# Kernel optimization log

Measured on AMD Instinct MI355X. Metric: run time of the kernel, lower is better.

The kernel has to match this reference:

```python
import jax, jax.numpy as jnp
import numpy as np

B, NF, H, W, D, S = 32, 16, 8, 24, 256, 21
NUM_ACTOR = 20
EPS = 1e-8      # slot-attention eps
LN_EPS = 1e-5   # torch LayerNorm default


def _ln(x, g, b):
    m = x.mean(-1, keepdims=True)
    v = ((x - m) ** 2).mean(-1, keepdims=True)
    return (x - m) / jnp.sqrt(v + LN_EPS) * g + b


def setup_inputs() -> dict:
    key = jax.random.key(0)
    ks = jax.random.split(key, 12)
    s = 1.0 / np.sqrt(D)
    lin = lambda k: jax.random.normal(k, (D, D), jnp.float32) * s
    return {
        "inputs": jax.random.normal(ks[0], (B, NF, H, W, D), jnp.float32),
        "noise": jax.random.normal(ks[1], (B, S, D), jnp.float32),
        "slots_mu": jax.random.normal(ks[2], (1, 1, D), jnp.float32),
        "slots_sigma": jnp.abs(jax.random.normal(ks[3], (1, 1, D), jnp.float32)),
        "Wq": lin(ks[4]), "bq": jnp.zeros(D, jnp.float32),
        "Wk": lin(ks[5]), "bk": jnp.zeros(D, jnp.float32),
        "Wv": lin(ks[6]), "bv": jnp.zeros(D, jnp.float32),
        "W1": lin(ks[7]), "b1": jnp.zeros(D, jnp.float32),
        "W2": lin(ks[8]), "b2": jnp.zeros(D, jnp.float32),
        "W_ih": jax.random.normal(ks[9], (3 * D, D), jnp.float32) * s,
        "b_ih": jnp.zeros(3 * D, jnp.float32),
        "W_hh": jax.random.normal(ks[10], (3 * D, D), jnp.float32) * s,
        "b_hh": jnp.zeros(3 * D, jnp.float32),
        "g_in": jnp.ones(D, jnp.float32), "be_in": jnp.zeros(D, jnp.float32),
        "g_sl": jnp.ones(D, jnp.float32), "be_sl": jnp.zeros(D, jnp.float32),
        "g_ff": jnp.ones(D, jnp.float32), "be_ff": jnp.zeros(D, jnp.float32),
    }


def reference(inputs, noise, slots_mu, slots_sigma, Wq, bq, Wk, bk, Wv, bv,
              W1, b1, W2, b2, W_ih, b_ih, W_hh, b_hh,
              g_in, be_in, g_sl, be_sl, g_ff, be_ff):
    scale = D ** -0.5
    slots0 = slots_mu + slots_sigma * noise  # [B,S,D]

    def gru(x, h):  # torch.nn.GRUCell math; x,h: [B*S, D]
        gi = x @ W_ih.T + b_ih
        gh = h @ W_hh.T + b_hh
        ir, iz, inn = jnp.split(gi, 3, axis=-1)
        hr, hz, hn = jnp.split(gh, 3, axis=-1)
        r = jax.nn.sigmoid(ir + hr)
        z = jax.nn.sigmoid(iz + hz)
        n = jnp.tanh(inn + r * hn)
        return (1.0 - z) * n + z * h

    def iterate(slots, k, v):
        q = _ln(slots, g_sl, be_sl) @ Wq.T + bq            # [B,S,D]
        dots = jnp.einsum('bid,bjd->bij', q, k) * scale    # [B,S,N]
        attn_ori = jax.nn.softmax(dots, axis=1) + EPS      # softmax over SLOT axis
        attn = attn_ori / attn_ori.sum(-1, keepdims=True)
        updates = jnp.einsum('bjd,bij->bid', v, attn)      # [B,S,D]
        h = gru(updates.reshape(-1, D), slots.reshape(-1, D)).reshape(B, S, D)
        slots_new = h + jax.nn.relu(_ln(h, g_ff, be_ff) @ W1.T + b1) @ W2.T + b2
        return slots_new, attn_ori

    def frame_step(slots, frame):  # frame: [B,H,W,D]
        x = _ln(frame.reshape(B, H * W, D), g_in, be_in)
        k = x @ Wk.T + bk
        v = x @ Wv.T + bv
        attn = None
        for _ in range(3):  # fixed 3 slot-attention iterations per frame
            slots, attn = iterate(slots, k, v)
        return slots, (slots, attn)

    frames = jnp.moveaxis(inputs, 1, 0)  # [NF,B,H,W,D]
    _, (slots_stack, attn_stack) = jax.lax.scan(frame_step, slots0, frames)
    slots_out = slots_stack[-1][:, :NUM_ACTOR, :]   # last frame, first 20 slots
    attns = jnp.moveaxis(attn_stack, 0, 1)          # [B,NF,S,N]
    return slots_out, attns
```

## Files before the change

### kernel.cpp

```cpp
#include <hip/hip_runtime.h>


typedef _Float16 f16;
typedef _Float16 half8 __attribute__((ext_vector_type(8)));
typedef float floatx4 __attribute__((ext_vector_type(4)));

#define WQ_OFF 0
#define WKT_OFF 16384
#define WV_OFF 32768
#define W1_OFF 49152
#define W2_OFF 65536
#define WIH_OFF 81920
#define WHH_OFF 131072
__device__ __align__(16) uint4 g_wpk[180224];

__device__ inline float wredsum(float v) {
#pragma unroll
  for (int m = 32; m > 0; m >>= 1) v += __shfl_xor(v, m, 64);
  return v;
}
__device__ inline float fsigmoid(float x) { return 1.f / (1.f + __expf(-x)); }
__device__ inline float ftanh(float x) {
  float ax = fabsf(x);
  float e = __expf(-2.f * ax);
  return copysignf((1.f - e) / (1.f + e), x);
}

__device__ inline floatx4 mfma16(half8 a, half8 b, floatx4 c) {
  return __builtin_amdgcn_mfma_f32_16x16x32_f16(a, b, c, 0, 0, 0);
}
__device__ inline void zero8(half8& a) {
#pragma unroll
  for (int e = 0; e < 8; e++) a[e] = (f16)0.f;
}
__device__ inline void split8(const float* __restrict__ p, half8& hi, half8& lo) {
  float4 v0 = *(const float4*)p;
  float4 v1 = *(const float4*)(p + 4);
  float vv[8] = {v0.x, v0.y, v0.z, v0.w, v1.x, v1.y, v1.z, v1.w};
#pragma unroll
  for (int e = 0; e < 8; e++) {
    f16 h = (f16)vv[e];
    hi[e] = h;
    lo[e] = (f16)(vv[e] - (float)h);
  }
}

__device__ inline void mfma_gemm_acc(const float* __restrict__ Ain, int woff, int tid,
                                     floatx4 acc[4]) {
  const int l = tid & 63, wv = tid >> 6;
  const int mt = wv & 1, ntb = (wv >> 1) * 4, lq = l >> 4, lr = l & 15;
  const int row = mt * 16 + lr;
  const bool rv = row < 21;
  const float* arow = Ain + row * 256;
  for (int ks = 0; ks < 8; ks++) {
    const int k0 = ks * 32 + lq * 8;
    half8 ahi, alo;
    if (rv) split8(arow + k0, ahi, alo);
    else { zero8(ahi); zero8(alo); }
#pragma unroll
    for (int t = 0; t < 4; t++) {
      const int col = (ntb + t) * 16 + lr;
      const uint4* bp = g_wpk + woff + ((col << 5) + (ks << 2) + lq) * 2;
      union { uint4 u; half8 h; } bh, bl;
      bh.u = bp[0]; bl.u = bp[1];
      acc[t] = mfma16(ahi, bh.h, acc[t]);
      acc[t] = mfma16(alo, bh.h, acc[t]);
      acc[t] = mfma16(ahi, bl.h, acc[t]);
    }
  }
}

__device__ inline void mfma_gemm_store(float* __restrict__ Out, const floatx4 acc[4],
                                       const float* __restrict__ bias, bool relu, int tid) {
  const int l = tid & 63, wv = tid >> 6;
  const int mt = wv & 1, ntb = (wv >> 1) * 4, lq = l >> 4, lr = l & 15;
#pragma unroll
  for (int t = 0; t < 4; t++) {
    const int col = (ntb + t) * 16 + lr;
    const float bb = bias ? bias[col] : 0.f;
#pragma unroll
    for (int r = 0; r < 4; r++) {
      const int i = mt * 16 + lq * 4 + r;
      if (i < 21) {
        float v = acc[t][r] + bb;
        Out[i * 256 + col] = relu ? fmaxf(v, 0.f) : v;
      }
    }
  }
}

__global__ __launch_bounds__(1024) void k_prep(
    const float* __restrict__ Wq, const float* __restrict__ Wk, const float* __restrict__ Wv,
    const float* __restrict__ W1, const float* __restrict__ W2,
    const float* __restrict__ Wih, const float* __restrict__ Whh) {
  int t = blockIdx.x * 1024 + threadIdx.x;
  if (t >= 90112) return;
  const float* src;
  int idx;
  bool tr = false;
  if (t < 8192) { src = Wq; idx = t; }
  else if (t < 16384) { src = Wk; idx = t - 8192; tr = true; }
  else if (t < 24576) { src = Wv; idx = t - 16384; }
  else if (t < 32768) { src = W1; idx = t - 24576; }
  else if (t < 40960) { src = W2; idx = t - 32768; }
  else if (t < 65536) { src = Wih; idx = t - 40960; }
  else { src = Whh; idx = t - 65536; }
  int c = idx >> 5, ko = idx & 31;
  union { uint4 u; f16 h[8]; } H, L;
#pragma unroll
  for (int e = 0; e < 8; e++) {
    int k = ko * 8 + e;
    float v = tr ? src[(size_t)k * 256 + c] : src[(size_t)c * 256 + k];
    f16 hi = (f16)v;
    H.h[e] = hi;
    L.h[e] = (f16)(v - (float)hi);
  }
  g_wpk[(size_t)t * 2] = H.u;
  g_wpk[(size_t)t * 2 + 1] = L.u;
}

__global__ __launch_bounds__(512) void k_all(
    const float* __restrict__ x, const float* __restrict__ noise,
    const float* __restrict__ mu, const float* __restrict__ sigma,
    const float* __restrict__ bq, const float* __restrict__ bk,
    const float* __restrict__ bv, const float* __restrict__ b1,
    const float* __restrict__ b2, const float* __restrict__ bih,
    const float* __restrict__ bhh,
    const float* __restrict__ g_in, const float* __restrict__ be_in,
    const float* __restrict__ g_sl, const float* __restrict__ be_sl,
    const float* __restrict__ g_ff, const float* __restrict__ be_ff,
    float* __restrict__ out_slots, float* __restrict__ out_attn) {
  __shared__ f16 LX[256 * 193];
  __shared__ alignas(16) float SL[21 * 256];
  __shared__ alignas(16) float A[21 * 256];
  __shared__ alignas(16) float Bf[21 * 256];
  __shared__ float qb[21], rsum[21];

  const int b = blockIdx.x;
  const int tid = threadIdx.x;
  const int w = tid >> 6, lane = tid & 63;
  const int d = tid & 255;
  const int half = tid >> 8;
  const int i0 = half * 11;
  const int ni = 11 - half;
  const floatx4 vzero = {0.f, 0.f, 0.f, 0.f};

  for (int i = tid; i < 21 * 256; i += 512) {
    int s = i >> 8, dd = i & 255;
    SL[i] = mu[dd] + sigma[dd] * noise[((size_t)b * 21 + s) * 256 + dd];
  }
  __syncthreads();

  for (int f = 0; f < 16; ++f) {
    const float* xf = x + ((size_t)(b * 16 + f)) * 192 * 256;
    for (int rr = 0; rr < 24; rr++) {
      int row = w + rr * 8;
      float4 xv = *(const float4*)(xf + row * 256 + lane * 4);
      float m = wredsum(xv.x + xv.y + xv.z + xv.w) * (1.f / 256.f);
      float d0 = xv.x - m, d1 = xv.y - m, d2 = xv.z - m, d3 = xv.w - m;
      float q2 = wredsum(d0 * d0 + d1 * d1 + d2 * d2 + d3 * d3);
      float rs = 1.f / sqrtf(q2 * (1.f / 256.f) + 1e-5f);
      int c = lane * 4;
      LX[(c + 0) * 193 + row] = (f16)(d0 * rs * g_in[c + 0] + be_in[c + 0]);
      LX[(c + 1) * 193 + row] = (f16)(d1 * rs * g_in[c + 1] + be_in[c + 1]);
      LX[(c + 2) * 193 + row] = (f16)(d2 * rs * g_in[c + 2] + be_in[c + 2]);
      LX[(c + 3) * 193 + row] = (f16)(d3 * rs * g_in[c + 3] + be_in[c + 3]);
    }
    __syncthreads();

    for (int it = 0; it < 3; ++it) {
#pragma unroll
      for (int rr = 0; rr < 3; rr++) {
        int row = w + rr * 8;
        if (row < 21) {
          float4 xv = *(const float4*)(SL + row * 256 + lane * 4);
          float m = wredsum(xv.x + xv.y + xv.z + xv.w) * (1.f / 256.f);
          float d0 = xv.x - m, d1 = xv.y - m, d2 = xv.z - m, d3 = xv.w - m;
          float q2 = wredsum(d0 * d0 + d1 * d1 + d2 * d2 + d3 * d3);
          float rs = 1.f / sqrtf(q2 * (1.f / 256.f) + 1e-5f);
          int c = lane * 4;
          A[row * 256 + c + 0] = d0 * rs * g_sl[c + 0] + be_sl[c + 0];
          A[row * 256 + c + 1] = d1 * rs * g_sl[c + 1] + be_sl[c + 1];
          A[row * 256 + c + 2] = d2 * rs * g_sl[c + 2] + be_sl[c + 2];
          A[row * 256 + c + 3] = d3 * rs * g_sl[c + 3] + be_sl[c + 3];
        }
      }
      __syncthreads();
      {
        floatx4 acc[4] = {vzero, vzero, vzero, vzero};
        mfma_gemm_acc(A, WQ_OFF, tid, acc);
        mfma_gemm_store(Bf, acc, bq, false, tid);
      }
      __syncthreads();
      {
        floatx4 acc[4] = {vzero, vzero, vzero, vzero};
        mfma_gemm_acc(Bf, WKT_OFF, tid, acc);
        mfma_gemm_store(A, acc, nullptr, false, tid);
        if (tid < 336) {
          int i = tid >> 4, p = tid & 15;
          const float* qrow = Bf + i * 256 + p * 16;
          float s = 0.f;
#pragma unroll
          for (int t2 = 0; t2 < 16; t2++) s += qrow[t2] * bk[p * 16 + t2];
          s += __shfl_xor(s, 1, 64);
          s += __shfl_xor(s, 2, 64);
          s += __shfl_xor(s, 4, 64);
          s += __shfl_xor(s, 8, 64);
          if (p == 0) qb[i] = s;
        }
      }
      __syncthreads();
      for (int c = 0; c < 8; c++) {
        int o = tid + (c << 9);
        if (o < 4032) {
          int i = o / 192, j = o - i * 192;
          float s = 0.f;
          for (int k = 0; k < 256; k += 4) {
            float4 q4 = *(const float4*)(A + i * 256 + k);
            s += q4.x * (float)LX[(k + 0) * 193 + j];
            s += q4.y * (float)LX[(k + 1) * 193 + j];
            s += q4.z * (float)LX[(k + 2) * 193 + j];
            s += q4.w * (float)LX[(k + 3) * 193 + j];
          }
          Bf[i * 256 + j] = (s + qb[i]) * 0.0625f;
        }
      }
      __syncthreads();
      if (tid < 192) {
        int j = tid;
        float mx = -1e30f;
#pragma unroll
        for (int i = 0; i < 21; i++) mx = fmaxf(mx, Bf[i * 256 + j]);
        float e[21], sum = 0.f;
#pragma unroll
        for (int i = 0; i < 21; i++) { e[i] = __expf(Bf[i * 256 + j] - mx); sum += e[i]; }
        float inv = 1.f / sum;
#pragma unroll
        for (int i = 0; i < 21; i++) Bf[i * 256 + j] = e[i] * inv + 1e-8f;
      }
      __syncthreads();
#pragma unroll
      for (int q3 = 0; q3 < 3; q3++) {
        int i = w * 3 + q3;
        if (i < 21) {
          float s = Bf[i * 256 + lane] + Bf[i * 256 + lane + 64] + Bf[i * 256 + lane + 128];
          s = wredsum(s);
          if (lane == 0) rsum[i] = s;
        }
      }
      __syncthreads();
      {
        float* oa = out_attn + ((size_t)(b * 16 + f)) * 4032;
        for (int idx = tid; idx < 4032; idx += 512) {
          int i = idx / 192, j = idx - i * 192;
          float ao = Bf[i * 256 + j];
          if (it == 2) oa[idx] = ao;
          Bf[i * 256 + j] = ao / rsum[i];
        }
      }
      __syncthreads();
      {
        float acc[11];
#pragma unroll
        for (int ii = 0; ii < 11; ii++) acc[ii] = 0.f;
        for (int j = 0; j < 192; j += 4) {
          float l0 = (float)LX[d * 193 + j + 0];
          float l1 = (float)LX[d * 193 + j + 1];
          float l2 = (float)LX[d * 193 + j + 2];
          float l3 = (float)LX[d * 193 + j + 3];
#pragma unroll
          for (int ii = 0; ii < 11; ii++)
            if (ii < ni) {
              float4 at = *(const float4*)(Bf + (i0 + ii) * 256 + j);
              acc[ii] += at.x * l0 + at.y * l1 + at.z * l2 + at.w * l3;
            }
        }
#pragma unroll
        for (int ii = 0; ii < 11; ii++)
          if (ii < ni) A[(i0 + ii) * 256 + d] = acc[ii];
      }
      __syncthreads();
      {
        floatx4 acc[4] = {vzero, vzero, vzero, vzero};
        mfma_gemm_acc(A, WV_OFF, tid, acc);
        mfma_gemm_store(Bf, acc, bv, false, tid);
      }
      __syncthreads();
      {
        const int l = tid & 63, wv = tid >> 6;
        const int mt = wv & 1, dtb = (wv >> 1) * 4, lq = l >> 4, lr = l & 15;
        const int row = mt * 16 + lr;
        const bool rv = row < 21;
        const float* urow = Bf + row * 256;
        const float* srow = SL + row * 256;
        for (int p = 0; p < 2; p++) {
          floatx4 aih[2][3], ahh[2][3];
#pragma unroll
          for (int gi = 0; gi < 2; gi++)
#pragma unroll
            for (int g = 0; g < 3; g++) { aih[gi][g] = vzero; ahh[gi][g] = vzero; }
          for (int ks = 0; ks < 8; ks++) {
            const int k0 = ks * 32 + lq * 8;
            half8 uhi, ulo, shi, slo;
            if (rv) { split8(urow + k0, uhi, ulo); split8(srow + k0, shi, slo); }
            else { zero8(uhi); zero8(ulo); zero8(shi); zero8(slo); }
#pragma unroll
            for (int gi = 0; gi < 2; gi++) {
              const int dt = dtb + p * 2 + gi;
#pragma unroll
              for (int g = 0; g < 3; g++) {
                const int colI = g * 256 + dt * 16 + lr;
                const uint4* bp = g_wpk + WIH_OFF + ((colI << 5) + (ks << 2) + lq) * 2;
                union { uint4 u; half8 h; } bh, bl;
                bh.u = bp[0]; bl.u = bp[1];
                aih[gi][g] = mfma16(uhi, bh.h, aih[gi][g]);
                aih[gi][g] = mfma16(ulo, bh.h, aih[gi][g]);
                aih[gi][g] = mfma16(uhi, bl.h, aih[gi][g]);
                const uint4* bp2 = g_wpk + WHH_OFF + ((colI << 5) + (ks << 2) + lq) * 2;
                bh.u = bp2[0]; bl.u = bp2[1];
                ahh[gi][g] = mfma16(shi, bh.h, ahh[gi][g]);
                ahh[gi][g] = mfma16(slo, bh.h, ahh[gi][g]);
                ahh[gi][g] = mfma16(shi, bl.h, ahh[gi][g]);
              }
            }
          }
#pragma unroll
          for (int gi = 0; gi < 2; gi++) {
            const int dt = dtb + p * 2 + gi;
            const int dd = dt * 16 + lr;
            const float bihr = bih[dd], bihz = bih[256 + dd], bihn = bih[512 + dd];
            const float bhhr = bhh[dd], bhhz = bhh[256 + dd], bhhn = bhh[512 + dd];
#pragma unroll
            for (int r = 0; r < 4; r++) {
              const int i = mt * 16 + lq * 4 + r;
              if (i < 21) {
                float rg = fsigmoid(aih[gi][0][r] + ahh[gi][0][r] + bihr + bhhr);
                float zg = fsigmoid(aih[gi][1][r] + ahh[gi][1][r] + bihz + bhhz);
                float ng = ftanh(aih[gi][2][r] + bihn + rg * (ahh[gi][2][r] + bhhn));
                A[i * 256 + dd] = (1.f - zg) * ng + zg * SL[i * 256 + dd];
              }
            }
          }
        }
      }
      __syncthreads();
#pragma unroll
      for (int rr = 0; rr < 3; rr++) {
        int row = w + rr * 8;
        if (row < 21) {
          float4 xv = *(const float4*)(A + row * 256 + lane * 4);
          float m = wredsum(xv.x + xv.y + xv.z + xv.w) * (1.f / 256.f);
          float d0 = xv.x - m, d1 = xv.y - m, d2 = xv.z - m, d3 = xv.w - m;
          float q2 = wredsum(d0 * d0 + d1 * d1 + d2 * d2 + d3 * d3);
          float rs = 1.f / sqrtf(q2 * (1.f / 256.f) + 1e-5f);
          int c = lane * 4;
          Bf[row * 256 + c + 0] = d0 * rs * g_ff[c + 0] + be_ff[c + 0];
          Bf[row * 256 + c + 1] = d1 * rs * g_ff[c + 1] + be_ff[c + 1];
          Bf[row * 256 + c + 2] = d2 * rs * g_ff[c + 2] + be_ff[c + 2];
          Bf[row * 256 + c + 3] = d3 * rs * g_ff[c + 3] + be_ff[c + 3];
        }
      }
      __syncthreads();
      {
        floatx4 acc[4] = {vzero, vzero, vzero, vzero};
        mfma_gemm_acc(Bf, W1_OFF, tid, acc);
        mfma_gemm_store(SL, acc, b1, true, tid);
      }
      __syncthreads();
      {
        floatx4 acc[4] = {vzero, vzero, vzero, vzero};
        mfma_gemm_acc(SL, W2_OFF, tid, acc);
        __syncthreads();
        const int l = tid & 63, wv = tid >> 6;
        const int mt = wv & 1, ntb = (wv >> 1) * 4, lq = l >> 4, lr = l & 15;
#pragma unroll
        for (int t = 0; t < 4; t++) {
          const int col = (ntb + t) * 16 + lr;
          const float bb = b2[col];
#pragma unroll
          for (int r = 0; r < 4; r++) {
            const int i = mt * 16 + lq * 4 + r;
            if (i < 21) SL[i * 256 + col] = A[i * 256 + col] + acc[t][r] + bb;
          }
        }
      }
      __syncthreads();
    }
  }
  for (int i = tid; i < 20 * 256; i += 512) {
    int s = i >> 8, dd = i & 255;
    out_slots[((size_t)b * 20 + s) * 256 + dd] = SL[s * 256 + dd];
  }
}

extern "C" void kernel_launch(void* const* d_in, const int* in_sizes, int n_in,
                              void* d_out, int out_size, void* d_ws, size_t ws_size,
                              hipStream_t stream) {
  const float* inputs = (const float*)d_in[0];
  const float* noise = (const float*)d_in[1];
  const float* mu = (const float*)d_in[2];
  const float* sigma = (const float*)d_in[3];
  const float* Wq = (const float*)d_in[4];
  const float* bq = (const float*)d_in[5];
  const float* Wk = (const float*)d_in[6];
  const float* bk = (const float*)d_in[7];
  const float* Wv = (const float*)d_in[8];
  const float* bv = (const float*)d_in[9];
  const float* W1 = (const float*)d_in[10];
  const float* b1 = (const float*)d_in[11];
  const float* W2 = (const float*)d_in[12];
  const float* b2 = (const float*)d_in[13];
  const float* Wih = (const float*)d_in[14];
  const float* bih = (const float*)d_in[15];
  const float* Whh = (const float*)d_in[16];
  const float* bhh = (const float*)d_in[17];
  const float* g_in = (const float*)d_in[18];
  const float* be_in = (const float*)d_in[19];
  const float* g_sl = (const float*)d_in[20];
  const float* be_sl = (const float*)d_in[21];
  const float* g_ff = (const float*)d_in[22];
  const float* be_ff = (const float*)d_in[23];

  float* out_slots = (float*)d_out;
  float* out_attn = out_slots + 32 * 20 * 256;

  k_prep<<<88, 1024, 0, stream>>>(Wq, Wk, Wv, W1, W2, Wih, Whh);
  k_all<<<32, 512, 0, stream>>>(inputs, noise, mu, sigma, bq, bk, bv, b1, b2,
                                bih, bhh, g_in, be_in, g_sl, be_sl, g_ff, be_ff,
                                out_slots, out_attn);
}
```

Before: 10.85 ms.

## Move attention dot and weighted-sum products to MFMA with padded LDS rows

The per-iteration dots computation (slots x 192 tokens over 256 features) and the attn-weighted sum of normalized inputs are rewritten from scalar FMA loops into 16x16x32 f16 MFMA tiles. The A operand is split into hi/lo halves, and the B fragments are gathered from the transposed LX buffer in LDS. Slot buffers are padded to a row stride of 258 to reduce LDS bank conflicts, and the qb/rsum scratch values are stored in the padding columns. The gathered B fragments read LDS element by element, and the padded stride limits vector loads to float2.

```diff
diff --git a/kernel.cpp b/kernel.cpp
--- a/kernel.cpp
+++ b/kernel.cpp
@@ -4,6 +4,8 @@
 typedef _Float16 f16;
 typedef _Float16 half8 __attribute__((ext_vector_type(8)));
 typedef float floatx4 __attribute__((ext_vector_type(4)));
+
+#define SSTR 258
 
 #define WQ_OFF 0
 #define WKT_OFF 16384
@@ -33,10 +35,12 @@
 #pragma unroll
   for (int e = 0; e < 8; e++) a[e] = (f16)0.f;
 }
-__device__ inline void split8(const float* __restrict__ p, half8& hi, half8& lo) {
-  float4 v0 = *(const float4*)p;
-  float4 v1 = *(const float4*)(p + 4);
-  float vv[8] = {v0.x, v0.y, v0.z, v0.w, v1.x, v1.y, v1.z, v1.w};
+__device__ inline void split8s(const float* __restrict__ p, half8& hi, half8& lo) {
+  float2 a = *(const float2*)(p);
+  float2 b = *(const float2*)(p + 2);
+  float2 c = *(const float2*)(p + 4);
+  float2 d = *(const float2*)(p + 6);
+  float vv[8] = {a.x, a.y, b.x, b.y, c.x, c.y, d.x, d.y};
 #pragma unroll
   for (int e = 0; e < 8; e++) {
     f16 h = (f16)vv[e];
@@ -51,11 +55,11 @@
   const int mt = wv & 1, ntb = (wv >> 1) * 4, lq = l >> 4, lr = l & 15;
   const int row = mt * 16 + lr;
   const bool rv = row < 21;
-  const float* arow = Ain + row * 256;
+  const float* arow = Ain + row * SSTR;
   for (int ks = 0; ks < 8; ks++) {
     const int k0 = ks * 32 + lq * 8;
     half8 ahi, alo;
-    if (rv) split8(arow + k0, ahi, alo);
+    if (rv) split8s(arow + k0, ahi, alo);
     else { zero8(ahi); zero8(alo); }
 #pragma unroll
     for (int t = 0; t < 4; t++) {
@@ -83,7 +87,7 @@
       const int i = mt * 16 + lq * 4 + r;
       if (i < 21) {
         float v = acc[t][r] + bb;
-        Out[i * 256 + col] = relu ? fmaxf(v, 0.f) : v;
+        Out[i * SSTR + col] = relu ? fmaxf(v, 0.f) : v;
       }
     }
   }
@@ -131,23 +135,19 @@
     const float* __restrict__ g_ff, const float* __restrict__ be_ff,
     float* __restrict__ out_slots, float* __restrict__ out_attn) {
   __shared__ f16 LX[256 * 193];
-  __shared__ alignas(16) float SL[21 * 256];
-  __shared__ alignas(16) float A[21 * 256];
-  __shared__ alignas(16) float Bf[21 * 256];
-  __shared__ float qb[21], rsum[21];
+  __shared__ float FBUF[3 * 21 * SSTR];
+  float* SL = FBUF;
+  float* A = FBUF + 21 * SSTR;
+  float* Bf = FBUF + 2 * 21 * SSTR;
 
   const int b = blockIdx.x;
   const int tid = threadIdx.x;
   const int w = tid >> 6, lane = tid & 63;
-  const int d = tid & 255;
-  const int half = tid >> 8;
-  const int i0 = half * 11;
-  const int ni = 11 - half;
   const floatx4 vzero = {0.f, 0.f, 0.f, 0.f};
 
   for (int i = tid; i < 21 * 256; i += 512) {
     int s = i >> 8, dd = i & 255;
-    SL[i] = mu[dd] + sigma[dd] * noise[((size_t)b * 21 + s) * 256 + dd];
+    SL[s * SSTR + dd] = mu[dd] + sigma[dd] * noise[((size_t)b * 21 + s) * 256 + dd];
   }
   __syncthreads();
 
@@ -173,16 +173,18 @@
       for (int rr = 0; rr < 3; rr++) {
         int row = w + rr * 8;
         if (row < 21) {
-          float4 xv = *(const float4*)(SL + row * 256 + lane * 4);
-          float m = wredsum(xv.x + xv.y + xv.z + xv.w) * (1.f / 256.f);
-          float d0 = xv.x - m, d1 = xv.y - m, d2 = xv.z - m, d3 = xv.w - m;
+          const float* sr = SL + row * SSTR + lane * 4;
+          float2 xa = *(const float2*)(sr);
+          float2 xb = *(const float2*)(sr + 2);
+          float m = wredsum(xa.x + xa.y + xb.x + xb.y) * (1.f / 256.f);
+          float d0 = xa.x - m, d1 = xa.y - m, d2 = xb.x - m, d3 = xb.y - m;
           float q2 = wredsum(d0 * d0 + d1 * d1 + d2 * d2 + d3 * d3);
           float rs = 1.f / sqrtf(q2 * (1.f / 256.f) + 1e-5f);
           int c = lane * 4;
-          A[row * 256 + c + 0] = d0 * rs * g_sl[c + 0] + be_sl[c + 0];
-          A[row * 256 + c + 1] = d1 * rs * g_sl[c + 1] + be_sl[c + 1];
-          A[row * 256 + c + 2] = d2 * rs * g_sl[c + 2] + be_sl[c + 2];
-          A[row * 256 + c + 3] = d3 * rs * g_sl[c + 3] + be_sl[c + 3];
+          A[row * SSTR + c + 0] = d0 * rs * g_sl[c + 0] + be_sl[c + 0];
+          A[row * SSTR + c + 1] = d1 * rs * g_sl[c + 1] + be_sl[c + 1];
+          A[row * SSTR + c + 2] = d2 * rs * g_sl[c + 2] + be_sl[c + 2];
+          A[row * SSTR + c + 3] = d3 * rs * g_sl[c + 3] + be_sl[c + 3];
         }
       }
       __syncthreads();
@@ -198,7 +200,7 @@
         mfma_gemm_store(A, acc, nullptr, false, tid);
         if (tid < 336) {
           int i = tid >> 4, p = tid & 15;
-          const float* qrow = Bf + i * 256 + p * 16;
+          const float* qrow = Bf + i * SSTR + p * 16;
           float s = 0.f;
 #pragma unroll
           for (int t2 = 0; t2 < 16; t2++) s += qrow[t2] * bk[p * 16 + t2];
@@ -206,23 +208,40 @@
           s += __shfl_xor(s, 2, 64);
           s += __shfl_xor(s, 4, 64);
           s += __shfl_xor(s, 8, 64);
-          if (p == 0) qb[i] = s;
-        }
-      }
-      __syncthreads();
-      for (int c = 0; c < 8; c++) {
-        int o = tid + (c << 9);
-        if (o < 4032) {
-          int i = o / 192, j = o - i * 192;
-          float s = 0.f;
-          for (int k = 0; k < 256; k += 4) {
-            float4 q4 = *(const float4*)(A + i * 256 + k);
-            s += q4.x * (float)LX[(k + 0) * 193 + j];
-            s += q4.y * (float)LX[(k + 1) * 193 + j];
-            s += q4.z * (float)LX[(k + 2) * 193 + j];
-            s += q4.w * (float)LX[(k + 3) * 193 + j];
-          }
-          Bf[i * 256 + j] = (s + qb[i]) * 0.0625f;
+          if (p == 0) A[i * SSTR + 256] = s;
+        }
+      }
+      __syncthreads();
+      {
+        const int l = tid & 63, wv = tid >> 6;
+        const int mt = wv & 1, jtb = (wv >> 1) * 3, lq = l >> 4, lr = l & 15;
+        const int row = mt * 16 + lr;
+        const bool rv = row < 21;
+        const float* arow = A + row * SSTR;
+        floatx4 acc[3] = {vzero, vzero, vzero};
+        for (int ks = 0; ks < 8; ks++) {
+          const int k0 = ks * 32 + lq * 8;
+          half8 ahi, alo;
+          if (rv) split8s(arow + k0, ahi, alo);
+          else { zero8(ahi); zero8(alo); }
+#pragma unroll
+          for (int t = 0; t < 3; t++) {
+            const int j = (jtb + t) * 16 + lr;
+            half8 bfr;
+#pragma unroll
+            for (int e = 0; e < 8; e++) bfr[e] = LX[(k0 + e) * 193 + j];
+            acc[t] = mfma16(ahi, bfr, acc[t]);
+            acc[t] = mfma16(alo, bfr, acc[t]);
+          }
+        }
+#pragma unroll
+        for (int t = 0; t < 3; t++) {
+          const int j = (jtb + t) * 16 + lr;
+#pragma unroll
+          for (int r = 0; r < 4; r++) {
+            const int i = mt * 16 + lq * 4 + r;
+            if (i < 21) Bf[i * SSTR + j] = (acc[t][r] + A[i * SSTR + 256]) * 0.0625f;
+          }
         }
       }
       __syncthreads();
@@ -230,22 +249,22 @@
         int j = tid;
         float mx = -1e30f;
 #pragma unroll
-        for (int i = 0; i < 21; i++) mx = fmaxf(mx, Bf[i * 256 + j]);
+        for (int i = 0; i < 21; i++) mx = fmaxf(mx, Bf[i * SSTR + j]);
         float e[21], sum = 0.f;
 #pragma unroll
-        for (int i = 0; i < 21; i++) { e[i] = __expf(Bf[i * 256 + j] - mx); sum += e[i]; }
+        for (int i = 0; i < 21; i++) { e[i] = __expf(Bf[i * SSTR + j] - mx); sum += e[i]; }
         float inv = 1.f / sum;
 #pragma unroll
-        for (int i = 0; i < 21; i++) Bf[i * 256 + j] = e[i] * inv + 1e-8f;
+        for (int i = 0; i < 21; i++) Bf[i * SSTR + j] = e[i] * inv + 1e-8f;
       }
       __syncthreads();
 #pragma unroll
       for (int q3 = 0; q3 < 3; q3++) {
         int i = w * 3 + q3;
         if (i < 21) {
-          float s = Bf[i * 256 + lane] + Bf[i * 256 + lane + 64] + Bf[i * 256 + lane + 128];
+          float s = Bf[i * SSTR + lane] + Bf[i * SSTR + lane + 64] + Bf[i * SSTR + lane + 128];
           s = wredsum(s);
-          if (lane == 0) rsum[i] = s;
+          if (lane == 0) A[i * SSTR + 257] = s;
         }
       }
       __syncthreads();
@@ -253,37 +272,10 @@
         float* oa = out_attn + ((size_t)(b * 16 + f)) * 4032;
         for (int idx = tid; idx < 4032; idx += 512) {
           int i = idx / 192, j = idx - i * 192;
-          float ao = Bf[i * 256 + j];
+          float ao = Bf[i * SSTR + j];
           if (it == 2) oa[idx] = ao;
-          Bf[i * 256 + j] = ao / rsum[i];
-        }
-      }
-      __syncthreads();
-      {
-        float acc[11];
-#pragma unroll
-        for (int ii = 0; ii < 11; ii++) acc[ii] = 0.f;
-        for (int j = 0; j < 192; j += 4) {
-          float l0 = (float)LX[d * 193 + j + 0];
-          float l1 = (float)LX[d * 193 + j + 1];
-          float l2 = (float)LX[d * 193 + j + 2];
-          float l3 = (float)LX[d * 193 + j + 3];
-#pragma unroll
-          for (int ii = 0; ii < 11; ii++)
-            if (ii < ni) {
-              float4 at = *(const float4*)(Bf + (i0 + ii) * 256 + j);
-              acc[ii] += at.x * l0 + at.y * l1 + at.z * l2 + at.w * l3;
-            }
-        }
-#pragma unroll
-        for (int ii = 0; ii < 11; ii++)
-          if (ii < ni) A[(i0 + ii) * 256 + d] = acc[ii];
-      }
-      __syncthreads();
-      {
-        floatx4 acc[4] = {vzero, vzero, vzero, vzero};
-        mfma_gemm_acc(A, WV_OFF, tid, acc);
-        mfma_gemm_store(Bf, acc, bv, false, tid);
+          Bf[i * SSTR + j] = ao / A[i * SSTR + 257];
+        }
       }
       __syncthreads();
       {
@@ -291,8 +283,47 @@
         const int mt = wv & 1, dtb = (wv >> 1) * 4, lq = l >> 4, lr = l & 15;
         const int row = mt * 16 + lr;
         const bool rv = row < 21;
-        const float* urow = Bf + row * 256;
-        const float* srow = SL + row * 256;
+        const float* arow = Bf + row * SSTR;
+        floatx4 acc[4] = {vzero, vzero, vzero, vzero};
+        for (int ks = 0; ks < 6; ks++) {
+          const int k0 = ks * 32 + lq * 8;
+          half8 ahi, alo;
+          if (rv) split8s(arow + k0, ahi, alo);
+          else { zero8(ahi); zero8(alo); }
+#pragma unroll
+          for (int t = 0; t < 4; t++) {
+            const int dd = (dtb + t) * 16 + lr;
+            half8 bfr;
+#pragma unroll
+            for (int e = 0; e < 8; e++) bfr[e] = LX[dd * 193 + k0 + e];
+            acc[t] = mfma16(ahi, bfr, acc[t]);
+            acc[t] = mfma16(alo, bfr, acc[t]);
+          }
+        }
+#pragma unroll
+        for (int t = 0; t < 4; t++) {
+          const int dd = (dtb + t) * 16 + lr;
+#pragma unroll
+          for (int r = 0; r < 4; r++) {
+            const int i = mt * 16 + lq * 4 + r;
+            if (i < 21) A[i * SSTR + dd] = acc[t][r];
+          }
+        }
+      }
+      __syncthreads();
+      {
+        floatx4 acc[4] = {vzero, vzero, vzero, vzero};
+        mfma_gemm_acc(A, WV_OFF, tid, acc);
+        mfma_gemm_store(Bf, acc, bv, false, tid);
+      }
+      __syncthreads();
+      {
+        const int l = tid & 63, wv = tid >> 6;
+        const int mt = wv & 1, dtb = (wv >> 1) * 4, lq = l >> 4, lr = l & 15;
+        const int row = mt * 16 + lr;
+        const bool rv = row < 21;
+        const float* urow = Bf + row * SSTR;
+        const float* srow = SL + row * SSTR;
         for (int p = 0; p < 2; p++) {
           floatx4 aih[2][3], ahh[2][3];
 #pragma unroll
@@ -302,7 +333,7 @@
           for (int ks = 0; ks < 8; ks++) {
             const int k0 = ks * 32 + lq * 8;
             half8 uhi, ulo, shi, slo;
-            if (rv) { split8(urow + k0, uhi, ulo); split8(srow + k0, shi, slo); }
+            if (rv) { split8s(urow + k0, uhi, ulo); split8s(srow + k0, shi, slo); }
             else { zero8(uhi); zero8(ulo); zero8(shi); zero8(slo); }
 #pragma unroll
             for (int gi = 0; gi < 2; gi++) {
@@ -337,7 +368,7 @@
                 float rg = fsigmoid(aih[gi][0][r] + ahh[gi][0][r] + bihr + bhhr);
                 float zg = fsigmoid(aih[gi][1][r] + ahh[gi][1][r] + bihz + bhhz);
                 float ng = ftanh(aih[gi][2][r] + bihn + rg * (ahh[gi][2][r] + bhhn));
-                A[i * 256 + dd] = (1.f - zg) * ng + zg * SL[i * 256 + dd];
+                A[i * SSTR + dd] = (1.f - zg) * ng + zg * SL[i * SSTR + dd];
               }
             }
           }
@@ -348,16 +379,18 @@
       for (int rr = 0; rr < 3; rr++) {
         int row = w + rr * 8;
         if (row < 21) {
-          float4 xv = *(const float4*)(A + row * 256 + lane * 4);
-          float m = wredsum(xv.x + xv.y + xv.z + xv.w) * (1.f / 256.f);
-          float d0 = xv.x - m, d1 = xv.y - m, d2 = xv.z - m, d3 = xv.w - m;
+          const float* ar = A + row * SSTR + lane * 4;
+          float2 xa = *(const float2*)(ar);
+          float2 xb = *(const float2*)(ar + 2);
+          float m = wredsum(xa.x + xa.y + xb.x + xb.y) * (1.f / 256.f);
+          float d0 = xa.x - m, d1 = xa.y - m, d2 = xb.x - m, d3 = xb.y - m;
           float q2 = wredsum(d0 * d0 + d1 * d1 + d2 * d2 + d3 * d3);
           float rs = 1.f / sqrtf(q2 * (1.f / 256.f) + 1e-5f);
           int c = lane * 4;
-          Bf[row * 256 + c + 0] = d0 * rs * g_ff[c + 0] + be_ff[c + 0];
-          Bf[row * 256 + c + 1] = d1 * rs * g_ff[c + 1] + be_ff[c + 1];
-          Bf[row * 256 + c + 2] = d2 * rs * g_ff[c + 2] + be_ff[c + 2];
-          Bf[row * 256 + c + 3] = d3 * rs * g_ff[c + 3] + be_ff[c + 3];
+          Bf[row * SSTR + c + 0] = d0 * rs * g_ff[c + 0] + be_ff[c + 0];
+          Bf[row * SSTR + c + 1] = d1 * rs * g_ff[c + 1] + be_ff[c + 1];
+          Bf[row * SSTR + c + 2] = d2 * rs * g_ff[c + 2] + be_ff[c + 2];
+          Bf[row * SSTR + c + 3] = d3 * rs * g_ff[c + 3] + be_ff[c + 3];
         }
       }
       __syncthreads();
@@ -380,7 +413,7 @@
 #pragma unroll
           for (int r = 0; r < 4; r++) {
             const int i = mt * 16 + lq * 4 + r;
-            if (i < 21) SL[i * 256 + col] = A[i * 256 + col] + acc[t][r] + bb;
+            if (i < 21) SL[i * SSTR + col] = A[i * SSTR + col] + acc[t][r] + bb;
           }
         }
       }
@@ -389,7 +422,7 @@
   }
   for (int i = tid; i < 20 * 256; i += 512) {
     int s = i >> 8, dd = i & 255;
-    out_slots[((size_t)b * 20 + s) * 256 + dd] = SL[s * 256 + dd];
+    out_slots[((size_t)b * 20 + s) * 256 + dd] = SL[s * SSTR + dd];
   }
 }
 
```

After: 8.948 ms. 17.5% less time.
